# Kernel tuning notes

Measured on AMD Instinct MI355X. Metric: run time of the kernel, lower is better.

Reference implementation:

```python
import jax, jax.numpy as jnp
import numpy as np

N = 512   # speakers
M = 64    # samples per speaker
D = 768   # embedding dim
EPS = 1e-8  # torch F.cosine_similarity eps


def setup_inputs() -> dict:
    key = jax.random.key(0)
    k1, = jax.random.split(key, 1)
    speaker_vectors = jax.random.normal(k1, (N * M, D), dtype=jnp.float32)
    w = jnp.asarray(10.0, dtype=jnp.float32)
    b = jnp.asarray(-5.0, dtype=jnp.float32)
    return {"speaker_vectors": speaker_vectors, "w": w, "b": b}


def _cosine(a, b):
    # torch F.cosine_similarity: a.b / (max(|a|,eps) * max(|b|,eps)), over last dim
    na = jnp.maximum(jnp.linalg.norm(a, axis=-1), EPS)
    nb = jnp.maximum(jnp.linalg.norm(b, axis=-1), EPS)
    return jnp.sum(a * b, axis=-1) / (na * nb)


def reference(speaker_vectors, w, b):
    x = speaker_vectors.reshape(N, M, D)            # [N, M, D]
    sums = x.sum(axis=1)                            # [N, D]
    centroids = sums / M                            # [N, D]
    excl = (sums[:, None, :] - x) / (M - 1)         # exclusive centroids [N, M, D]

    # cosine sim of every centroid against every sample: [N_centroid, N_spk, M]
    xn = jnp.maximum(jnp.linalg.norm(x, axis=-1), EPS)          # [N, M]
    cn = jnp.maximum(jnp.linalg.norm(centroids, axis=-1), EPS)  # [N]
    dots = jnp.einsum('nd,imd->nim', centroids, x)              # [N, N, M]
    S = w * (dots / (cn[:, None, None] * xn[None])) + b         # [N, N, M]

    # same-speaker entries use the leave-one-out centroid
    S_same = w * _cosine(excl, x) + b               # [N, M]
    idx = jnp.arange(N)
    S = S.at[idx, idx].set(S_same)                  # overwrite diagonal block

    # L_j = -S_same_j + log sum_n exp(S[n, j])
    L = -S_same + jax.scipy.special.logsumexp(S, axis=0)  # [N, M]
    return L.sum()
```

## Files before the change

kernel.cpp:

```cpp
#include <hip/hip_runtime.h>
#include <hip/hip_bf16.h>
#include <math.h>

#define EPS 1e-8f

typedef __attribute__((ext_vector_type(2))) unsigned long ulongx2;
typedef __attribute__((ext_vector_type(4))) float floatx4;
typedef unsigned char uchar_t;

#define GPTR(p) ((const __attribute__((address_space(1))) void*)(p))
#define LPTR(p) ((__attribute__((address_space(3))) void*)(p))

__device__ __forceinline__ unsigned int pk4(float a, float b, float c, float d) {
  int v = __builtin_amdgcn_cvt_pk_fp8_f32(a, b, 0, false);
  v = __builtin_amdgcn_cvt_pk_fp8_f32(c, d, v, true);
  return (unsigned int)v;
}

__global__ __launch_bounds__(256) void kA(const float* __restrict__ x,
    uchar_t* __restrict__ xbf8fm, float* __restrict__ sums_f32,
    float* __restrict__ xx, float* __restrict__ rxn) {
  const int g = blockIdx.x;
  const int n = g >> 2;
  const int t = threadIdx.x;
  const int wv = t >> 6, l = t & 63;
  __shared__ uchar_t xs[16][776];
  __shared__ float csum[4][768];
  float4 cs0 = {0,0,0,0}, cs1 = {0,0,0,0}, cs2 = {0,0,0,0};

#pragma unroll
  for (int rr = 0; rr < 4; ++rr) {
    const int r = wv * 4 + rr;
    const size_t base = ((size_t)g * 16 + r) * 768;
    const float* rp = x + base;
    float4 v0 = *(const float4*)(rp + l * 4);
    float4 v1 = *(const float4*)(rp + l * 4 + 256);
    float4 v2 = *(const float4*)(rp + l * 4 + 512);
    *(unsigned int*)&xs[r][l * 4]       = pk4(v0.x, v0.y, v0.z, v0.w);
    *(unsigned int*)&xs[r][l * 4 + 256] = pk4(v1.x, v1.y, v1.z, v1.w);
    *(unsigned int*)&xs[r][l * 4 + 512] = pk4(v2.x, v2.y, v2.z, v2.w);
    float rq = v0.x*v0.x + v0.y*v0.y + v0.z*v0.z + v0.w*v0.w
             + v1.x*v1.x + v1.y*v1.y + v1.z*v1.z + v1.w*v1.w
             + v2.x*v2.x + v2.y*v2.y + v2.z*v2.z + v2.w*v2.w;
    for (int o = 32; o; o >>= 1) rq += __shfl_xor(rq, o, 64);
    if (l == 0) {
      const int j = g * 16 + r;
      xx[j] = rq;
      rxn[j] = 1.0f / fmaxf(sqrtf(rq), EPS);
    }
    cs0.x += v0.x; cs0.y += v0.y; cs0.z += v0.z; cs0.w += v0.w;
    cs1.x += v1.x; cs1.y += v1.y; cs1.z += v1.z; cs1.w += v1.w;
    cs2.x += v2.x; cs2.y += v2.y; cs2.z += v2.z; cs2.w += v2.w;
  }
  *(float4*)&csum[wv][l * 4]       = cs0;
  *(float4*)&csum[wv][l * 4 + 256] = cs1;
  *(float4*)&csum[wv][l * 4 + 512] = cs2;
  __syncthreads();

#pragma unroll
  for (int q = 0; q < 3; ++q) {
    const int c = t + q * 256;
    const float s = csum[0][c] + csum[1][c] + csum[2][c] + csum[3][c];
    atomicAdd(&sums_f32[(size_t)n * 768 + c], s);
  }

#pragma unroll
  for (int ksi = 0; ksi < 3; ++ksi) {
    const int ks = wv * 3 + ksi;
    const uchar_t* sp = &xs[l & 15][ks * 64 + (l >> 4) * 8];
    uint2 lo = *(const uint2*)sp;
    uint2 hi = *(const uint2*)(sp + 32);
    uint4 outv = {lo.x, lo.y, hi.x, hi.y};
    *(uint4*)(xbf8fm + (size_t)((g * 12 + ks) * 64 + l) * 16) = outv;
  }
}

__global__ __launch_bounds__(256) void kA2(const float* __restrict__ sums_f32,
    uchar_t* __restrict__ sums8fm, float* __restrict__ ss,
    float* __restrict__ rcn, const float* __restrict__ wp) {
  const int g = blockIdx.x;
  const int wv = threadIdx.x >> 6, l = threadIdx.x & 63;
#pragma unroll
  for (int ksi = 0; ksi < 3; ++ksi) {
    const int ks = wv * 3 + ksi;
    const float* sp = sums_f32 + (size_t)(g * 16 + (l & 15)) * 768
                      + ks * 64 + (l >> 4) * 8;
    float4 a0 = *(const float4*)sp;
    float4 a1 = *(const float4*)(sp + 4);
    float4 b0 = *(const float4*)(sp + 32);
    float4 b1 = *(const float4*)(sp + 36);
    uint4 outv = { pk4(a0.x, a0.y, a0.z, a0.w), pk4(a1.x, a1.y, a1.z, a1.w),
                   pk4(b0.x, b0.y, b0.z, b0.w), pk4(b1.x, b1.y, b1.z, b1.w) };
    *(uint4*)(sums8fm + (size_t)((g * 12 + ks) * 64 + l) * 16) = outv;
  }
#pragma unroll
  for (int sp4 = 0; sp4 < 4; ++sp4) {
    const int n = g * 16 + wv * 4 + sp4;
    const float* spt = sums_f32 + (size_t)n * 768;
    float4 u0 = *(const float4*)(spt + l * 4);
    float4 u1 = *(const float4*)(spt + l * 4 + 256);
    float4 u2 = *(const float4*)(spt + l * 4 + 512);
    float lss = u0.x*u0.x + u0.y*u0.y + u0.z*u0.z + u0.w*u0.w
              + u1.x*u1.x + u1.y*u1.y + u1.z*u1.z + u1.w*u1.w
              + u2.x*u2.x + u2.y*u2.y + u2.z*u2.z + u2.w*u2.w;
    for (int o = 32; o; o >>= 1) lss += __shfl_xor(lss, o, 64);
    if (l == 0) {
      ss[n] = lss;
      rcn[n] = (*wp) / fmaxf(sqrtf(lss), 64.f * EPS);
    }
  }
}

__global__ __launch_bounds__(512, 2) void kC(const uchar_t* __restrict__ xbf8fm,
    const uchar_t* __restrict__ sums8fm, const float* __restrict__ rcn,
    const float* __restrict__ rxn, float* __restrict__ colsum,
    float* __restrict__ sdiag_dot, const float* __restrict__ bp) {
  __shared__ uchar_t lds[4][32768];
  const int b = blockIdx.x;
  const int xcd = b & 7;
  const int inner = b >> 3;
  const int nt = inner & 1;
  const int jt = xcd + ((inner >> 1) << 3);
  const int n0 = nt * 256, j0 = jt * 256;
  const int t = threadIdx.x, wv = t >> 6, l = t & 63;
  const int wm = wv >> 2, wj = wv & 3;
  const int gA0 = n0 / 16, gB0 = j0 / 16;

#define STAGE(KS_, BUF_) {                                                     \
    const int fb0_ = wv * 2, fb1_ = wv * 2 + 1;                                \
    __builtin_amdgcn_global_load_lds(                                          \
        GPTR(sums8fm + (size_t)(((gA0 + fb0_) * 12 + (KS_)) * 64 + l) * 16),   \
        LPTR(&lds[BUF_][fb0_ * 1024]), 16, 0, 0);                              \
    __builtin_amdgcn_global_load_lds(                                          \
        GPTR(sums8fm + (size_t)(((gA0 + fb1_) * 12 + (KS_)) * 64 + l) * 16),   \
        LPTR(&lds[BUF_][fb1_ * 1024]), 16, 0, 0);                              \
    __builtin_amdgcn_global_load_lds(                                          \
        GPTR(xbf8fm + (size_t)(((gB0 + fb0_) * 12 + (KS_)) * 64 + l) * 16),    \
        LPTR(&lds[BUF_][16384 + fb0_ * 1024]), 16, 0, 0);                      \
    __builtin_amdgcn_global_load_lds(                                          \
        GPTR(xbf8fm + (size_t)(((gB0 + fb1_) * 12 + (KS_)) * 64 + l) * 16),    \
        LPTR(&lds[BUF_][16384 + fb1_ * 1024]), 16, 0, 0);                      \
  }

  floatx4 acc[8][4];
#pragma unroll
  for (int mi = 0; mi < 8; ++mi)
#pragma unroll
    for (int ni = 0; ni < 4; ++ni) acc[mi][ni] = (floatx4){0.f, 0.f, 0.f, 0.f};

  STAGE(0, 0)
  STAGE(1, 1)
  STAGE(2, 2)

  for (int kb = 0; kb < 12; ++kb) {
    if (kb < 10)       { asm volatile("s_waitcnt vmcnt(8)" ::: "memory"); }
    else if (kb == 10) { asm volatile("s_waitcnt vmcnt(4)" ::: "memory"); }
    else               { asm volatile("s_waitcnt vmcnt(0)" ::: "memory"); }
    __builtin_amdgcn_s_barrier();
    __builtin_amdgcn_sched_barrier(0);
    const int cb = kb & 3, sb = (kb + 3) & 3;

    ulongx2 af[8], bf[4];
#pragma unroll
    for (int ni = 0; ni < 4; ++ni)
      bf[ni] = *(const ulongx2*)&lds[cb][16384 + (wj * 4 + ni) * 1024 + l * 16];
#pragma unroll
    for (int mi = 0; mi < 8; ++mi)
      af[mi] = *(const ulongx2*)&lds[cb][(wm * 8 + mi) * 1024 + l * 16];
    if (kb + 3 < 12) STAGE(kb + 3, sb)
    __builtin_amdgcn_s_setprio(1);
#pragma unroll
    for (int mi = 0; mi < 8; ++mi)
#pragma unroll
      for (int ni = 0; ni < 4; ++ni) {
        acc[mi][ni] = __builtin_amdgcn_mfma_f32_16x16x32_fp8_fp8(
            (long)af[mi].x, (long)bf[ni].x, acc[mi][ni], 0, 0, 0);
        acc[mi][ni] = __builtin_amdgcn_mfma_f32_16x16x32_fp8_fp8(
            (long)af[mi].y, (long)bf[ni].y, acc[mi][ni], 0, 0, 0);
      }
    __builtin_amdgcn_s_setprio(0);
  }

  const float bb = *bp;
  float rxv[4], p[4] = {0.f, 0.f, 0.f, 0.f};
#pragma unroll
  for (int ni = 0; ni < 4; ++ni)
    rxv[ni] = rxn[j0 + wj * 64 + ni * 16 + (l & 15)];
  const bool diagblk = (nt == (jt >> 6));

#pragma unroll
  for (int mi = 0; mi < 8; ++mi) {
    float4 rr = *(const float4*)&rcn[n0 + wm * 128 + mi * 16 + ((l >> 4) << 2)];
    const float rc[4] = {rr.x, rr.y, rr.z, rr.w};
#pragma unroll
    for (int ni = 0; ni < 4; ++ni) {
      floatx4 a = acc[mi][ni];
#pragma unroll
      for (int q = 0; q < 4; ++q)
        p[ni] += __expf(a[q] * rc[q] * rxv[ni] + bb);
      if (diagblk) {
        const int jg = j0 + wj * 64 + ni * 16 + (l & 15);
#pragma unroll
        for (int q = 0; q < 4; ++q) {
          const int mg = n0 + wm * 128 + mi * 16 + ((l >> 4) << 2) + q;
          if (mg == (jg >> 6)) sdiag_dot[jg] = a[q];
        }
      }
    }
  }
#pragma unroll
  for (int ni = 0; ni < 4; ++ni) {
    p[ni] += __shfl_xor(p[ni], 16, 64);
    p[ni] += __shfl_xor(p[ni], 32, 64);
  }
  if (l < 16) {
#pragma unroll
    for (int ni = 0; ni < 4; ++ni)
      atomicAdd(&colsum[j0 + wj * 64 + ni * 16 + l], p[ni]);
  }
}

__global__ __launch_bounds__(256) void kD(const float* __restrict__ colsum,
    const float* __restrict__ sdiag_dot, const float* __restrict__ xx,
    const float* __restrict__ ss, const float* __restrict__ rcn,
    const float* __restrict__ wp, const float* __restrict__ bp,
    float* __restrict__ out) {
  const int j = blockIdx.x * 256 + threadIdx.x;
  const int i = j >> 6;
  const float ww = *wp, bb = *bp;
  const float sx = sdiag_dot[j];
  const float xxv = xx[j];
  const float xn = fmaxf(sqrtf(xxv), EPS);
  const float rx = 1.0f / xn;
  const float sd = sx * rcn[i] * rx + bb;
  const float exn = sqrtf(fmaxf(ss[i] - 2.f * sx + xxv, 0.f)) * (1.f / 63.f);
  const float edot = (sx - xxv) * (1.f / 63.f);
  const float sm = ww * edot / (fmaxf(exn, EPS) * xn) + bb;
  const float tot = colsum[j] - __expf(sd) + __expf(sm);
  float L = -sm + logf(fmaxf(tot, 1e-30f));
  for (int o = 32; o; o >>= 1) L += __shfl_xor(L, o, 64);
  __shared__ float red[4];
  if ((threadIdx.x & 63) == 0) red[threadIdx.x >> 6] = L;
  __syncthreads();
  if (threadIdx.x == 0) atomicAdd(out, red[0] + red[1] + red[2] + red[3]);
}

extern "C" void kernel_launch(void* const* d_in, const int* in_sizes, int n_in,
                              void* d_out, int out_size, void* d_ws, size_t ws_size,
                              hipStream_t stream) {
  const float* x  = (const float*)d_in[0];
  const float* wp = (const float*)d_in[1];
  const float* bp = (const float*)d_in[2];
  float* out = (float*)d_out;

  float* fws = (float*)d_ws;
  float* ss        = fws;
  float* rcn       = fws + 512;
  float* xx        = fws + 1024;
  float* rxn       = fws + 33792;
  float* colsum    = fws + 66560;
  float* sdiag_dot = fws + 99328;
  float* sums_f32  = fws + 132096;
  uchar_t* sums8fm = (uchar_t*)(fws + 525312);
  uchar_t* xbf8fm  = (uchar_t*)(fws + 623616);

  hipMemsetAsync(colsum, 0, 32768 * sizeof(float), stream);
  hipMemsetAsync(sums_f32, 0, 393216 * sizeof(float), stream);
  hipMemsetAsync(out, 0, sizeof(float), stream);

  kA<<<2048, 256, 0, stream>>>(x, xbf8fm, sums_f32, xx, rxn);
  kA2<<<32, 256, 0, stream>>>(sums_f32, sums8fm, ss, rcn, wp);
  kC<<<256, 512, 0, stream>>>(xbf8fm, sums8fm, rcn, rxn, colsum, sdiag_dot, bp);
  kD<<<128, 256, 0, stream>>>(colsum, sdiag_dot, xx, ss, rcn, wp, bp, out);
}
```

Measured before the change: 63.21 us.

## Replace global atomic speaker sums with per-block partials reduced in kA2

kA no longer atomically adds column sums into a zeroed global sums buffer. Each block now reduces its 16 rows through LDS atomics and writes a plain partial row, and kA2 sums four partials per speaker into shared memory, then computes norms and the fp8 packing from there. This removes the memset of the sums buffer and the contended global float atomics. In exchange, kA2 reads four times as much partial data with only 32 blocks, and the workspace layout grows.

```diff
diff --git a/kernel.cpp b/kernel.cpp
--- a/kernel.cpp
+++ b/kernel.cpp
@@ -18,16 +18,18 @@
 }
 
 __global__ __launch_bounds__(256) void kA(const float* __restrict__ x,
-    uchar_t* __restrict__ xbf8fm, float* __restrict__ sums_f32,
+    uchar_t* __restrict__ xbf8fm, float* __restrict__ part,
     float* __restrict__ xx, float* __restrict__ rxn) {
   const int g = blockIdx.x;
-  const int n = g >> 2;
   const int t = threadIdx.x;
   const int wv = t >> 6, l = t & 63;
   __shared__ uchar_t xs[16][776];
-  __shared__ float csum[4][768];
+  __shared__ float csumL[768];
+
+  csumL[t] = 0.f; csumL[t + 256] = 0.f; csumL[t + 512] = 0.f;
+  __syncthreads();
+
   float4 cs0 = {0,0,0,0}, cs1 = {0,0,0,0}, cs2 = {0,0,0,0};
-
 #pragma unroll
   for (int rr = 0; rr < 4; ++rr) {
     const int r = wv * 4 + rr;
@@ -52,17 +54,17 @@
     cs1.x += v1.x; cs1.y += v1.y; cs1.z += v1.z; cs1.w += v1.w;
     cs2.x += v2.x; cs2.y += v2.y; cs2.z += v2.z; cs2.w += v2.w;
   }
-  *(float4*)&csum[wv][l * 4]       = cs0;
-  *(float4*)&csum[wv][l * 4 + 256] = cs1;
-  *(float4*)&csum[wv][l * 4 + 512] = cs2;
-  __syncthreads();
-
-#pragma unroll
-  for (int q = 0; q < 3; ++q) {
-    const int c = t + q * 256;
-    const float s = csum[0][c] + csum[1][c] + csum[2][c] + csum[3][c];
-    atomicAdd(&sums_f32[(size_t)n * 768 + c], s);
-  }
+  atomicAdd(&csumL[l * 4 + 0], cs0.x); atomicAdd(&csumL[l * 4 + 1], cs0.y);
+  atomicAdd(&csumL[l * 4 + 2], cs0.z); atomicAdd(&csumL[l * 4 + 3], cs0.w);
+  atomicAdd(&csumL[l * 4 + 256], cs1.x); atomicAdd(&csumL[l * 4 + 257], cs1.y);
+  atomicAdd(&csumL[l * 4 + 258], cs1.z); atomicAdd(&csumL[l * 4 + 259], cs1.w);
+  atomicAdd(&csumL[l * 4 + 512], cs2.x); atomicAdd(&csumL[l * 4 + 513], cs2.y);
+  atomicAdd(&csumL[l * 4 + 514], cs2.z); atomicAdd(&csumL[l * 4 + 515], cs2.w);
+  __syncthreads();
+
+  part[(size_t)g * 768 + t]       = csumL[t];
+  part[(size_t)g * 768 + t + 256] = csumL[t + 256];
+  part[(size_t)g * 768 + t + 512] = csumL[t + 512];
 
 #pragma unroll
   for (int ksi = 0; ksi < 3; ++ksi) {
@@ -75,16 +77,53 @@
   }
 }
 
-__global__ __launch_bounds__(256) void kA2(const float* __restrict__ sums_f32,
+__global__ __launch_bounds__(256) void kA2(const float* __restrict__ part,
     uchar_t* __restrict__ sums8fm, float* __restrict__ ss,
     float* __restrict__ rcn, const float* __restrict__ wp) {
   const int g = blockIdx.x;
-  const int wv = threadIdx.x >> 6, l = threadIdx.x & 63;
+  const int t = threadIdx.x;
+  const int wv = t >> 6, l = t & 63;
+  __shared__ float sums_l[16][772];
+  __shared__ float ssl[16];
+  if (t < 16) ssl[t] = 0.f;
+
+  float lss[16];
+#pragma unroll
+  for (int s = 0; s < 16; ++s) lss[s] = 0.f;
+#pragma unroll
+  for (int s = 0; s < 16; ++s) {
+    const int n = g * 16 + s;
+    const float* p0 = part + (size_t)(4 * n + 0) * 768;
+    const float* p1 = part + (size_t)(4 * n + 1) * 768;
+    const float* p2 = part + (size_t)(4 * n + 2) * 768;
+    const float* p3 = part + (size_t)(4 * n + 3) * 768;
+#pragma unroll
+    for (int q = 0; q < 3; ++q) {
+      const int c = t + q * 256;
+      const float v = p0[c] + p1[c] + p2[c] + p3[c];
+      sums_l[s][c] = v;
+      lss[s] += v * v;
+    }
+  }
+  __syncthreads();
+#pragma unroll
+  for (int s = 0; s < 16; ++s) {
+    float v = lss[s];
+    for (int o = 32; o; o >>= 1) v += __shfl_xor(v, o, 64);
+    if (l == 0) atomicAdd(&ssl[s], v);
+  }
+  __syncthreads();
+  if (t < 16) {
+    const int n = g * 16 + t;
+    const float v = ssl[t];
+    ss[n] = v;
+    rcn[n] = (*wp) / fmaxf(sqrtf(v), 64.f * EPS);
+  }
+
 #pragma unroll
   for (int ksi = 0; ksi < 3; ++ksi) {
     const int ks = wv * 3 + ksi;
-    const float* sp = sums_f32 + (size_t)(g * 16 + (l & 15)) * 768
-                      + ks * 64 + (l >> 4) * 8;
+    const float* sp = &sums_l[l & 15][ks * 64 + (l >> 4) * 8];
     float4 a0 = *(const float4*)sp;
     float4 a1 = *(const float4*)(sp + 4);
     float4 b0 = *(const float4*)(sp + 32);
@@ -92,22 +131,6 @@
     uint4 outv = { pk4(a0.x, a0.y, a0.z, a0.w), pk4(a1.x, a1.y, a1.z, a1.w),
                    pk4(b0.x, b0.y, b0.z, b0.w), pk4(b1.x, b1.y, b1.z, b1.w) };
     *(uint4*)(sums8fm + (size_t)((g * 12 + ks) * 64 + l) * 16) = outv;
-  }
-#pragma unroll
-  for (int sp4 = 0; sp4 < 4; ++sp4) {
-    const int n = g * 16 + wv * 4 + sp4;
-    const float* spt = sums_f32 + (size_t)n * 768;
-    float4 u0 = *(const float4*)(spt + l * 4);
-    float4 u1 = *(const float4*)(spt + l * 4 + 256);
-    float4 u2 = *(const float4*)(spt + l * 4 + 512);
-    float lss = u0.x*u0.x + u0.y*u0.y + u0.z*u0.z + u0.w*u0.w
-              + u1.x*u1.x + u1.y*u1.y + u1.z*u1.z + u1.w*u1.w
-              + u2.x*u2.x + u2.y*u2.y + u2.z*u2.z + u2.w*u2.w;
-    for (int o = 32; o; o >>= 1) lss += __shfl_xor(lss, o, 64);
-    if (l == 0) {
-      ss[n] = lss;
-      rcn[n] = (*wp) / fmaxf(sqrtf(lss), 64.f * EPS);
-    }
   }
 }
 
@@ -260,16 +283,15 @@
   float* rxn       = fws + 33792;
   float* colsum    = fws + 66560;
   float* sdiag_dot = fws + 99328;
-  float* sums_f32  = fws + 132096;
-  uchar_t* sums8fm = (uchar_t*)(fws + 525312);
-  uchar_t* xbf8fm  = (uchar_t*)(fws + 623616);
+  float* part      = fws + 132096;
+  uchar_t* sums8fm = (uchar_t*)(fws + 1704960);
+  uchar_t* xbf8fm  = (uchar_t*)(fws + 1803264);
 
   hipMemsetAsync(colsum, 0, 32768 * sizeof(float), stream);
-  hipMemsetAsync(sums_f32, 0, 393216 * sizeof(float), stream);
   hipMemsetAsync(out, 0, sizeof(float), stream);
 
-  kA<<<2048, 256, 0, stream>>>(x, xbf8fm, sums_f32, xx, rxn);
-  kA2<<<32, 256, 0, stream>>>(sums_f32, sums8fm, ss, rcn, wp);
+  kA<<<2048, 256, 0, stream>>>(x, xbf8fm, part, xx, rxn);
+  kA2<<<32, 256, 0, stream>>>(part, sums8fm, ss, rcn, wp);
   kC<<<256, 512, 0, stream>>>(xbf8fm, sums8fm, rcn, rxn, colsum, sdiag_dot, bp);
   kD<<<128, 256, 0, stream>>>(colsum, sdiag_dot, xx, ss, rcn, wp, bp, out);
 }
```

Result: slower. 92.29 us (+46.0%).
